# Performance work log

Measured on AMD Instinct MI355X. Metric: run time of the kernel, lower is better.

Reference implementation:

```python
import jax, jax.numpy as jnp
import numpy as np

N_INPUT, N_HIDDEN, N_OUTPUT = 64, 512, 24

def setup_inputs() -> dict:
    key = jax.random.key(0)
    ks = jax.random.split(key, 7)
    s_ih = 1.0 / np.sqrt(N_HIDDEN)
    x = jax.random.normal(ks[0], (256, 512, N_INPUT), dtype=jnp.float32)
    W_ih = jax.random.uniform(ks[1], (N_HIDDEN, N_INPUT), minval=-s_ih, maxval=s_ih, dtype=jnp.float32)
    W_hh = jax.random.uniform(ks[2], (N_HIDDEN, N_HIDDEN), minval=-s_ih, maxval=s_ih, dtype=jnp.float32)
    b_ih = jax.random.uniform(ks[3], (N_HIDDEN,), minval=-s_ih, maxval=s_ih, dtype=jnp.float32)
    b_hh = jax.random.uniform(ks[4], (N_HIDDEN,), minval=-s_ih, maxval=s_ih, dtype=jnp.float32)
    W_ho = jax.random.uniform(ks[5], (N_OUTPUT, N_HIDDEN), minval=-s_ih, maxval=s_ih, dtype=jnp.float32)
    b_ho = jax.random.uniform(ks[6], (N_OUTPUT,), minval=-s_ih, maxval=s_ih, dtype=jnp.float32)
    return {"x": x, "W_ih": W_ih, "W_hh": W_hh, "b_ih": b_ih, "b_hh": b_hh, "W_ho": W_ho, "b_ho": b_ho}

def reference(x, W_ih, W_hh, b_ih, b_hh, W_ho, b_ho):
    B = x.shape[0]
    # Precompute input projections for all timesteps in one big GEMM: [B,T,H]
    xp = jnp.einsum('bti,hi->bth', x, W_ih) + b_ih + b_hh
    h0 = jnp.zeros((B, W_hh.shape[0]), dtype=x.dtype)

    def step(h, xp_t):
        h = jnp.tanh(xp_t + h @ W_hh.T)
        out = jnp.tanh(h @ W_ho.T + b_ho)
        return h, out

    _, outs = jax.lax.scan(step, h0, jnp.swapaxes(xp, 0, 1))  # outs: [T,B,O]
    return jnp.swapaxes(outs, 0, 1)  # [B,T,O]
```

## Files before the change

kernel.cpp:

```cpp
#include <hip/hip_runtime.h>
#include <cstdint>
#include <cstddef>


#define TSTEPS 512
#define HDIM   512
#define NIN    64
#define NOUT   24
#define BB     16
#define HPAD   520
#define XPAD   72
#define KHALF  256
#define HPAD2  264
#define NREG   49
#define NLDS   (64 - NREG)

typedef _Float16 h16;
typedef __attribute__((ext_vector_type(8))) _Float16 h16x8;
typedef __attribute__((ext_vector_type(4))) _Float16 h16x4;
typedef __attribute__((ext_vector_type(2))) _Float16 h16x2;
typedef __attribute__((ext_vector_type(4))) float    f32x4;
typedef __attribute__((ext_vector_type(2))) float    f32x2;

__device__ __forceinline__ float fast_tanh(float z) {
  float e = __builtin_amdgcn_exp2f(z * 2.8853900817779268f);
  return 1.0f - 2.0f * __builtin_amdgcn_rcpf(e + 1.0f);
}

__device__ __forceinline__ h16x8 cvt8(const float* __restrict__ p) {
  f32x4 f0 = *(const f32x4*)p;
  f32x4 f1 = *(const f32x4*)(p + 4);
  h16x8 a;
  #pragma unroll
  for (int j = 0; j < 4; ++j) { a[j] = (h16)f0[j]; a[4 + j] = (h16)f1[j]; }
  return a;
}

__global__ __launch_bounds__(512)
void xp_gemm(const float* __restrict__ x, const float* __restrict__ Wih,
             const float* __restrict__ bih, const float* __restrict__ bhh,
             h16* __restrict__ xp, unsigned* __restrict__ cnt)
{
  const int tid  = threadIdx.x;
  const int wave = tid >> 6;
  const int lane = tid & 63;
  const int lr   = lane & 15;
  const int lk   = lane >> 4;
  const int blk  = blockIdx.x & 15;
  const int tc   = blockIdx.x >> 4;
  const int c0   = wave * 64;

  if (cnt && blockIdx.x == 0 && tid < 64) cnt[tid] = 0u;

  h16x8 A[4][2];
  #pragma unroll
  for (int m = 0; m < 4; ++m)
    #pragma unroll
    for (int s = 0; s < 2; ++s)
      A[m][s] = cvt8(Wih + (size_t)(c0 + 16 * m + lr) * NIN + 32 * s + 8 * lk);

  f32x4 bias[4];
  #pragma unroll
  for (int m = 0; m < 4; ++m) {
    const int c = c0 + 16 * m + 4 * lk;
    f32x4 bi = *(const f32x4*)&bih[c];
    f32x4 bh = *(const f32x4*)&bhh[c];
    bias[m] = bi + bh;
  }

  const float* xrow = x + (size_t)(16 * blk + lr) * (TSTEPS * NIN);

  for (int j = 0; j < 32; ++j) {
    const int t = tc * 32 + j;
    f32x4 acc[4];
    #pragma unroll
    for (int m = 0; m < 4; ++m) acc[m] = bias[m];
    #pragma unroll
    for (int s = 0; s < 2; ++s) {
      h16x8 bx = cvt8(xrow + (size_t)t * NIN + 32 * s + 8 * lk);
      #pragma unroll
      for (int m = 0; m < 4; ++m)
        acc[m] = __builtin_amdgcn_mfma_f32_16x16x32_f16(A[m][s], bx, acc[m], 0, 0, 0);
    }
    h16x8 c0v, c1v;
    #pragma unroll
    for (int i = 0; i < 4; ++i) {
      c0v[i]     = (h16)acc[0][i];
      c0v[4 + i] = (h16)acc[1][i];
      c1v[i]     = (h16)acc[2][i];
      c1v[4 + i] = (h16)acc[3][i];
    }
    h16* p = xp + ((((size_t)t * 16 + blk) * 8 + wave) * 64 + lane) * 16;
    *(h16x8*)p       = c0v;
    *(h16x8*)(p + 8) = c1v;
  }
}

__global__ __launch_bounds__(512, 2)
void rnn_core2(const float* __restrict__ Whh, const h16* __restrict__ xp,
               h16* __restrict__ hall, float* __restrict__ ex,
               unsigned* __restrict__ cnt)
{
  __shared__ h16 hl[2][16 * HPAD2];

  const int tid  = threadIdx.x;
  const int wave = tid >> 6;
  const int lane = tid & 63;
  const int lr   = lane & 15;
  const int lk   = lane >> 4;
  const int kb   = blockIdx.x >> 4;
  const int g    = blockIdx.x & 15;
  const int wq   = wave & 3;
  const bool fin = ((wave >> 2) == kb);
  const int b0   = g * 16;

  h16x8 areg[8][4];
  #pragma unroll
  for (int s = 0; s < 8; ++s)
    #pragma unroll
    for (int m = 0; m < 4; ++m)
      areg[s][m] = cvt8(Whh + (size_t)(64 * wave + 16 * m + lr) * HDIM
                        + KHALF * kb + 32 * s + 8 * lk);

  for (int idx = tid; idx < 16 * HPAD2; idx += 512) hl[0][idx] = (h16)0.f;
  __syncthreads();

  h16x8 xr0, xr1;
  if (fin) {
    const h16* p = xp + (((size_t)g * 8 + wave) * 64 + lane) * 16;
    xr0 = *(const h16x8*)p;
    xr1 = *(const h16x8*)(p + 8);
  }

  unsigned* mycnt   = &cnt[g * 2 + kb];
  unsigned* partcnt = &cnt[g * 2 + (1 - kb)];

  for (int t = 0; t < TSTEPS; ++t) {
    f32x4 acc[4];
    if (fin) {
      #pragma unroll
      for (int i = 0; i < 4; ++i) {
        acc[0][i] = (float)xr0[i];
        acc[1][i] = (float)xr0[4 + i];
        acc[2][i] = (float)xr1[i];
        acc[3][i] = (float)xr1[4 + i];
      }
      const int tn = (t + 1 < TSTEPS) ? (t + 1) : t;
      const h16* p = xp + ((((size_t)tn * 16 + g) * 8 + wave) * 64 + lane) * 16;
      xr0 = *(const h16x8*)p;
      xr1 = *(const h16x8*)(p + 8);
    } else {
      #pragma unroll
      for (int m = 0; m < 4; ++m) { acc[m][0]=0.f; acc[m][1]=0.f; acc[m][2]=0.f; acc[m][3]=0.f; }
    }

    const h16* hb = hl[t & 1];
    #pragma unroll
    for (int s = 0; s < 8; ++s) {
      h16x8 bh = *(const h16x8*)&hb[lr * HPAD2 + 32 * s + 8 * lk];
      #pragma unroll
      for (int m = 0; m < 4; ++m)
        acc[m] = __builtin_amdgcn_mfma_f32_16x16x32_f16(areg[s][m], bh, acc[m], 0, 0, 0);
    }

    if (!fin) {
      float* exw = ex + ((size_t)((g * 2 + kb) * 2 + (t & 1)) << 12);
      #pragma unroll
      for (int m = 0; m < 4; ++m)
        *(f32x4*)&exw[((wq * 16 + m * 4 + lk) << 6) + lr * 4] = acc[m];
      if (lane == 0)
        __hip_atomic_fetch_add(mycnt, 1u, __ATOMIC_RELEASE, __HIP_MEMORY_SCOPE_AGENT);
    } else {
      const unsigned tgt = 4u * (unsigned)(t + 1);
      while (__hip_atomic_load(partcnt, __ATOMIC_ACQUIRE, __HIP_MEMORY_SCOPE_AGENT) < tgt)
        __builtin_amdgcn_s_sleep(1);
      const float* exr = ex + ((size_t)((g * 2 + (1 - kb)) * 2 + (t & 1)) << 12);
      h16* hn   = hl[(t + 1) & 1];
      h16* hrow = hall + ((size_t)t * 256 + b0 + lr) * HDIM + KHALF * kb + 64 * wq + 4 * lk;
      #pragma unroll
      for (int m = 0; m < 4; ++m) {
        f32x4 pp = *(const f32x4*)&exr[((wq * 16 + m * 4 + lk) << 6) + lr * 4];
        h16x4 hv;
        #pragma unroll
        for (int i = 0; i < 4; ++i) hv[i] = (h16)fast_tanh(acc[m][i] + pp[i]);
        *(h16x4*)&hn[lr * HPAD2 + 64 * wq + 16 * m + 4 * lk] = hv;
        *(h16x4*)(hrow + 16 * m) = hv;
      }
    }

    __syncthreads();
  }
}

__global__ __launch_bounds__(512)
void out_all(const h16* __restrict__ hall, const float* __restrict__ Who,
             const float* __restrict__ bho, float* __restrict__ out)
{
  __shared__ h16 wholds[NOUT * HPAD];

  const int tid  = threadIdx.x;
  const int wave = tid >> 6;
  const int lane = tid & 63;
  const int lr   = lane & 15;
  const int lk   = lane >> 4;

  for (int idx = tid; idx < NOUT * HDIM; idx += 512) {
    int r = idx >> 9, k = idx & 511;
    wholds[r * HPAD + k] = (h16)Who[idx];
  }

  f32x4 o0, o1;
  { o0 = *(const f32x4*)&bho[lk * 4]; }
  { int ob = 16 + lk * 4;
    if (ob < NOUT) o1 = *(const f32x4*)&bho[ob];
    else { o1[0] = 0.f; o1[1] = 0.f; o1[2] = 0.f; o1[3] = 0.f; } }
  __syncthreads();

  const int rt = blockIdx.x * 8 + wave;
  const int t  = rt >> 4;
  const int b  = (rt & 15) * 16 + lr;
  const int row1 = (16 + lr < NOUT) ? (16 + lr) : (8 + lr);

  const h16* hrow = hall + ((size_t)t * 256 + b) * HDIM + lk * 8;

  #pragma unroll
  for (int s = 0; s < 16; ++s) {
    h16x8 bh = *(const h16x8*)(hrow + 32 * s);
    h16x8 a0 = *(const h16x8*)&wholds[lr * HPAD + s * 32 + lk * 8];
    h16x8 a1 = *(const h16x8*)&wholds[row1 * HPAD + s * 32 + lk * 8];
    o0 = __builtin_amdgcn_mfma_f32_16x16x32_f16(a0, bh, o0, 0, 0, 0);
    o1 = __builtin_amdgcn_mfma_f32_16x16x32_f16(a1, bh, o1, 0, 0, 0);
  }

  float* op = out + ((size_t)b * TSTEPS + t) * NOUT;
  f32x4 v0;
  #pragma unroll
  for (int i = 0; i < 4; ++i) v0[i] = fast_tanh(o0[i]);
  *(f32x4*)(op + lk * 4) = v0;
  if (lk < 2) {
    f32x4 v1;
    #pragma unroll
    for (int i = 0; i < 4; ++i) v1[i] = fast_tanh(o1[i]);
    *(f32x4*)(op + 16 + lk * 4) = v1;
  }
}

__global__ __launch_bounds__(512, 2)
void rnn_core(const float* __restrict__ Whh, const h16* __restrict__ xp,
              h16* __restrict__ hall)
{
  __shared__ h16 hbuf[2][BB * HPAD];
  __shared__ h16 aslice[NLDS * 8 * 512];

  const int tid  = threadIdx.x;
  const int wave = tid >> 6;
  const int lane = tid & 63;
  const int lr   = lane & 15;
  const int lk   = lane >> 4;
  const int blk  = blockIdx.x;
  const int b0   = blk * BB;
  const int wc0  = wave * 64;

  h16x8 areg[NREG];
  #pragma unroll
  for (int s = 0; s < 16; ++s) {
    #pragma unroll
    for (int m = 0; m < 4; ++m) {
      h16x8 a = cvt8(Whh + (size_t)(wc0 + 16 * m + lr) * HDIM + 32 * s + 8 * lk);
      const int id = s * 4 + m;
      if (id < NREG) areg[id] = a;
      else *(h16x8*)&aslice[(size_t)((id - NREG) * 8 + wave) * 512 + lane * 8] = a;
    }
  }

  for (int idx = tid; idx < BB * HPAD; idx += 512) hbuf[0][idx] = (h16)0.f;
  __syncthreads();

  h16x8 xr0, xr1;
  {
    const h16* p = xp + (((size_t)blk * 8 + wave) * 64 + lane) * 16;
    xr0 = *(const h16x8*)p;
    xr1 = *(const h16x8*)(p + 8);
  }

  for (int t = 0; t < TSTEPS; ++t) {
    const h16* hb = hbuf[t & 1];
    h16*       hn = hbuf[(t + 1) & 1];

    f32x4 acc[4];
    #pragma unroll
    for (int i = 0; i < 4; ++i) {
      acc[0][i] = (float)xr0[i];
      acc[1][i] = (float)xr0[4 + i];
      acc[2][i] = (float)xr1[i];
      acc[3][i] = (float)xr1[4 + i];
    }
    {
      const int tn = (t + 1 < TSTEPS) ? (t + 1) : t;
      const h16* p = xp + ((((size_t)tn * 16 + blk) * 8 + wave) * 64 + lane) * 16;
      xr0 = *(const h16x8*)p;
      xr1 = *(const h16x8*)(p + 8);
    }

    #pragma unroll
    for (int s = 0; s < 16; ++s) {
      h16x8 bh = *(const h16x8*)&hb[lr * HPAD + 32 * s + 8 * lk];
      #pragma unroll
      for (int m = 0; m < 4; ++m) {
        const int id = s * 4 + m;
        h16x8 a = (id < NREG)
            ? areg[id]
            : *(const h16x8*)&aslice[(size_t)((id - NREG) * 8 + wave) * 512 + lane * 8];
        acc[m] = __builtin_amdgcn_mfma_f32_16x16x32_f16(a, bh, acc[m], 0, 0, 0);
      }
    }

    h16* hrow = hall + ((size_t)t * 256 + b0 + lr) * HDIM + wc0 + lk * 4;
    #pragma unroll
    for (int m = 0; m < 4; ++m) {
      h16x4 hv;
      #pragma unroll
      for (int i = 0; i < 4; ++i) hv[i] = (h16)fast_tanh(acc[m][i]);
      *(h16x4*)&hn[lr * HPAD + wc0 + 16 * m + 4 * lk] = hv;
      *(h16x4*)(hrow + 16 * m) = hv;
    }

    __syncthreads();
  }
}

__device__ __forceinline__ void out_proj(
    int t, const h16* __restrict__ hb, const h16* __restrict__ who,
    f32x4 bho0, f32x4 bho1, float* __restrict__ out, int b0, int lr, int lk)
{
  f32x4 o0 = bho0, o1 = bho1;
  const int row1 = (16 + lr < NOUT) ? (16 + lr) : (8 + lr);
  #pragma unroll
  for (int s = 0; s < 16; ++s) {
    h16x8 bh = *(const h16x8*)&hb[lr * HPAD + s * 32 + lk * 8];
    h16x8 a0 = *(const h16x8*)&who[lr * HPAD + s * 32 + lk * 8];
    h16x8 a1 = *(const h16x8*)&who[row1 * HPAD + s * 32 + lk * 8];
    o0 = __builtin_amdgcn_mfma_f32_16x16x32_f16(a0, bh, o0, 0, 0, 0);
    o1 = __builtin_amdgcn_mfma_f32_16x16x32_f16(a1, bh, o1, 0, 0, 0);
  }
  float* op = out + ((size_t)(b0 + lr) * TSTEPS + t) * NOUT;
  f32x4 v0;
  #pragma unroll
  for (int i = 0; i < 4; ++i) v0[i] = fast_tanh(o0[i]);
  *(f32x4*)(op + lk * 4) = v0;
  if (lk < 2) {
    f32x4 v1;
    #pragma unroll
    for (int i = 0; i < 4; ++i) v1[i] = fast_tanh(o1[i]);
    *(f32x4*)(op + 16 + lk * 4) = v1;
  }
}

__global__ __launch_bounds__(512, 2)
void rnn_fused(const float* __restrict__ x,
               const float* __restrict__ Wih,
               const float* __restrict__ Whh,
               const float* __restrict__ bih,
               const float* __restrict__ bhh,
               const float* __restrict__ Who,
               const float* __restrict__ bho,
               float* __restrict__ out)
{
  __shared__ h16 hbuf[2][BB * HPAD];
  __shared__ h16 xbuf[2][BB * XPAD];
  __shared__ h16 wholds[NOUT * HPAD];

  const int tid  = threadIdx.x;
  const int wave = tid >> 6;
  const int lane = tid & 63;
  const int lr   = lane & 15;
  const int lk   = lane >> 4;
  const int b0   = blockIdx.x * BB;
  const int wc0  = wave * 64;

  h16x8 a_rec[4][16];
  #pragma unroll
  for (int m = 0; m < 4; ++m) {
    const int row = wc0 + m * 16 + lr;
    #pragma unroll
    for (int s = 0; s < 16; ++s)
      a_rec[m][s] = cvt8(Whh + (size_t)row * HDIM + s * 32 + lk * 8);
  }
  h16x8 a_ih[4][2];
  #pragma unroll
  for (int m = 0; m < 4; ++m) {
    const int row = wc0 + m * 16 + lr;
    #pragma unroll
    for (int s = 0; s < 2; ++s)
      a_ih[m][s] = cvt8(Wih + (size_t)row * NIN + s * 32 + lk * 8);
  }
  f32x4 biasv[4];
  #pragma unroll
  for (int m = 0; m < 4; ++m) {
    const int c = wc0 + m * 16 + lk * 4;
    f32x4 bi = *(const f32x4*)&bih[c];
    f32x4 bh2 = *(const f32x4*)&bhh[c];
    biasv[m] = bi + bh2;
  }
  f32x4 bho0, bho1;
  { bho0 = *(const f32x4*)&bho[lk * 4]; }
  { int ob = 16 + lk * 4;
    if (ob < NOUT) bho1 = *(const f32x4*)&bho[ob];
    else { bho1[0] = 0.f; bho1[1] = 0.f; bho1[2] = 0.f; bho1[3] = 0.f; } }

  for (int idx = tid; idx < NOUT * HDIM; idx += 512) {
    int r = idx >> 9, k = idx & 511;
    wholds[r * HPAD + k] = (h16)Who[idx];
  }
  for (int idx = tid; idx < BB * HPAD; idx += 512) hbuf[0][idx] = (h16)0.f;
  {
    int r = tid >> 5, c2 = (tid & 31) * 2;
    f32x2 v = *(const f32x2*)(x + ((size_t)(b0 + r) * TSTEPS + 0) * NIN + c2);
    h16x2 pk = { (h16)v.x, (h16)v.y };
    *(h16x2*)&xbuf[0][r * XPAD + c2] = pk;
  }
  __syncthreads();

  for (int t = 0; t < TSTEPS; ++t) {
    const h16* hb = hbuf[t & 1];
    h16*       hn = hbuf[(t + 1) & 1];
    const h16* xb = xbuf[t & 1];
    h16*       xn = xbuf[(t + 1) & 1];

    if (t > 0 && wave == ((t - 1) & 7))
      out_proj(t - 1, hb, wholds, bho0, bho1, out, b0, lr, lk);

    const int tl = (t + 1 < TSTEPS) ? (t + 1) : (TSTEPS - 1);
    const int xr = tid >> 5, xc = (tid & 31) * 2;
    f32x2 xv = *(const f32x2*)(x + ((size_t)(b0 + xr) * TSTEPS + tl) * NIN + xc);

    f32x4 acc[4];
    #pragma unroll
    for (int m = 0; m < 4; ++m) acc[m] = biasv[m];
    #pragma unroll
    for (int s = 0; s < 2; ++s) {
      h16x8 bx = *(const h16x8*)&xb[lr * XPAD + s * 32 + lk * 8];
      #pragma unroll
      for (int m = 0; m < 4; ++m)
        acc[m] = __builtin_amdgcn_mfma_f32_16x16x32_f16(a_ih[m][s], bx, acc[m], 0, 0, 0);
    }
    #pragma unroll
    for (int s = 0; s < 16; ++s) {
      h16x8 bh = *(const h16x8*)&hb[lr * HPAD + 32 * s + 8 * lk];
      #pragma unroll
      for (int m = 0; m < 4; ++m)
        acc[m] = __builtin_amdgcn_mfma_f32_16x16x32_f16(a_rec[m][s], bh, acc[m], 0, 0, 0);
    }
    #pragma unroll
    for (int m = 0; m < 4; ++m) {
      h16x4 hv;
      #pragma unroll
      for (int i = 0; i < 4; ++i) hv[i] = (h16)fast_tanh(acc[m][i]);
      *(h16x4*)&hn[lr * HPAD + wc0 + 16 * m + 4 * lk] = hv;
    }
    {
      h16x2 pk = { (h16)xv.x, (h16)xv.y };
      *(h16x2*)&xn[xr * XPAD + xc] = pk;
    }
    __syncthreads();
  }

  if (wave == ((TSTEPS - 1) & 7))
    out_proj(TSTEPS - 1, hbuf[TSTEPS & 1], wholds, bho0, bho1, out, b0, lr, lk);
}

extern "C" void kernel_launch(void* const* d_in, const int* in_sizes, int n_in,
                              void* d_out, int out_size, void* d_ws, size_t ws_size,
                              hipStream_t stream) {
  (void)in_sizes; (void)n_in; (void)out_size;
  const float* x   = (const float*)d_in[0];
  const float* Wih = (const float*)d_in[1];
  const float* Whh = (const float*)d_in[2];
  const float* bih = (const float*)d_in[3];
  const float* bhh = (const float*)d_in[4];
  const float* Who = (const float*)d_in[5];
  const float* bho = (const float*)d_in[6];
  float* out = (float*)d_out;

  const size_t XP_BYTES   = (size_t)TSTEPS * 256 * HDIM * sizeof(h16);
  const size_t HALL_BYTES = (size_t)TSTEPS * 256 * HDIM * sizeof(h16);
  const size_t EX_BYTES   = (size_t)64 * 4096 * sizeof(float);
  const size_t CNT_BYTES  = 64 * sizeof(unsigned);

  if (ws_size >= XP_BYTES + HALL_BYTES + EX_BYTES + CNT_BYTES) {
    h16*      xp   = (h16*)d_ws;
    h16*      hall = (h16*)((char*)d_ws + XP_BYTES);
    float*    ex   = (float*)((char*)d_ws + XP_BYTES + HALL_BYTES);
    unsigned* cnt  = (unsigned*)((char*)d_ws + XP_BYTES + HALL_BYTES + EX_BYTES);
    xp_gemm<<<dim3(256), dim3(512), 0, stream>>>(x, Wih, bih, bhh, xp, cnt);
    rnn_core2<<<dim3(32), dim3(512), 0, stream>>>(Whh, xp, hall, ex, cnt);
    out_all<<<dim3(1024), dim3(512), 0, stream>>>(hall, Who, bho, out);
  } else if (ws_size >= XP_BYTES + HALL_BYTES) {
    h16* xp   = (h16*)d_ws;
    h16* hall = (h16*)((char*)d_ws + XP_BYTES);
    xp_gemm<<<dim3(256), dim3(512), 0, stream>>>(x, Wih, bih, bhh, xp, nullptr);
    rnn_core<<<dim3(256 / BB), dim3(512), 0, stream>>>(Whh, xp, hall);
    out_all<<<dim3(1024), dim3(512), 0, stream>>>(hall, Who, bho, out);
  } else {
    rnn_fused<<<dim3(256 / BB), dim3(512), 0, stream>>>(x, Wih, Whh, bih, bhh, Who, bho, out);
  }
}
```

Measured before the change: 1.090 ms.

## Place exchange scratch in output tail and defer per-step hidden-state stores

The cross-block exchange buffer and sync counters for the split-K recurrence kernel now live in the tail of the output buffer instead of the workspace. This lets the two-block-per-group path run whenever the workspace holds only xp and hall. That tail is later fully overwritten by the output projection kernel. The global store of each step's hidden state is also deferred to the start of the next step, taking that store off the critical path before the barrier. The trade-off is that correctness now relies on the output buffer being large enough and on the kernels running in stream order.

```diff
diff --git a/kernel.cpp b/kernel.cpp
--- a/kernel.cpp
+++ b/kernel.cpp
@@ -14,6 +14,8 @@
 #define HPAD2  264
 #define NREG   49
 #define NLDS   (64 - NREG)
+#define EX_F32  (64 * 4096)
+#define CNT_U32 64
 
 typedef _Float16 h16;
 typedef __attribute__((ext_vector_type(8))) _Float16 h16x8;
@@ -50,7 +52,7 @@
   const int tc   = blockIdx.x >> 4;
   const int c0   = wave * 64;
 
-  if (cnt && blockIdx.x == 0 && tid < 64) cnt[tid] = 0u;
+  if (cnt && blockIdx.x == 0 && tid < CNT_U32) cnt[tid] = 0u;
 
   h16x8 A[4][2];
   #pragma unroll
@@ -135,7 +137,16 @@
   unsigned* mycnt   = &cnt[g * 2 + kb];
   unsigned* partcnt = &cnt[g * 2 + (1 - kb)];
 
+  h16x4 pend[4];
+  h16*  pendRow = hall;
+
   for (int t = 0; t < TSTEPS; ++t) {
+    if (fin && t > 0) {
+      #pragma unroll
+      for (int m = 0; m < 4; ++m)
+        *(h16x4*)(pendRow + 16 * m) = pend[m];
+    }
+
     f32x4 acc[4];
     if (fin) {
       #pragma unroll
@@ -175,8 +186,7 @@
       while (__hip_atomic_load(partcnt, __ATOMIC_ACQUIRE, __HIP_MEMORY_SCOPE_AGENT) < tgt)
         __builtin_amdgcn_s_sleep(1);
       const float* exr = ex + ((size_t)((g * 2 + (1 - kb)) * 2 + (t & 1)) << 12);
-      h16* hn   = hl[(t + 1) & 1];
-      h16* hrow = hall + ((size_t)t * 256 + b0 + lr) * HDIM + KHALF * kb + 64 * wq + 4 * lk;
+      h16* hn = hl[(t + 1) & 1];
       #pragma unroll
       for (int m = 0; m < 4; ++m) {
         f32x4 pp = *(const f32x4*)&exr[((wq * 16 + m * 4 + lk) << 6) + lr * 4];
@@ -184,11 +194,18 @@
         #pragma unroll
         for (int i = 0; i < 4; ++i) hv[i] = (h16)fast_tanh(acc[m][i] + pp[i]);
         *(h16x4*)&hn[lr * HPAD2 + 64 * wq + 16 * m + 4 * lk] = hv;
-        *(h16x4*)(hrow + 16 * m) = hv;
+        pend[m] = hv;
       }
+      pendRow = hall + ((size_t)t * 256 + b0 + lr) * HDIM + KHALF * kb + 64 * wq + 4 * lk;
     }
 
     __syncthreads();
+  }
+
+  if (fin) {
+    #pragma unroll
+    for (int m = 0; m < 4; ++m)
+      *(h16x4*)(pendRow + 16 * m) = pend[m];
   }
 }
 
@@ -472,7 +489,7 @@
 extern "C" void kernel_launch(void* const* d_in, const int* in_sizes, int n_in,
                               void* d_out, int out_size, void* d_ws, size_t ws_size,
                               hipStream_t stream) {
-  (void)in_sizes; (void)n_in; (void)out_size;
+  (void)in_sizes; (void)n_in;
   const float* x   = (const float*)d_in[0];
   const float* Wih = (const float*)d_in[1];
   const float* Whh = (const float*)d_in[2];
@@ -484,14 +501,13 @@
 
   const size_t XP_BYTES   = (size_t)TSTEPS * 256 * HDIM * sizeof(h16);
   const size_t HALL_BYTES = (size_t)TSTEPS * 256 * HDIM * sizeof(h16);
-  const size_t EX_BYTES   = (size_t)64 * 4096 * sizeof(float);
-  const size_t CNT_BYTES  = 64 * sizeof(unsigned);
-
-  if (ws_size >= XP_BYTES + HALL_BYTES + EX_BYTES + CNT_BYTES) {
+  const int    EX_TAIL    = EX_F32 + CNT_U32;
+
+  if (ws_size >= XP_BYTES + HALL_BYTES && out_size >= EX_TAIL + 16) {
     h16*      xp   = (h16*)d_ws;
     h16*      hall = (h16*)((char*)d_ws + XP_BYTES);
-    float*    ex   = (float*)((char*)d_ws + XP_BYTES + HALL_BYTES);
-    unsigned* cnt  = (unsigned*)((char*)d_ws + XP_BYTES + HALL_BYTES + EX_BYTES);
+    float*    ex   = out + ((size_t)out_size - EX_TAIL);
+    unsigned* cnt  = (unsigned*)(ex + EX_F32);
     xp_gemm<<<dim3(256), dim3(512), 0, stream>>>(x, Wih, bih, bhh, xp, cnt);
     rnn_core2<<<dim3(32), dim3(512), 0, stream>>>(Whh, xp, hall, ex, cnt);
     out_all<<<dim3(1024), dim3(512), 0, stream>>>(hall, Who, bho, out);
```

Measured after the change: 3.759 ms. 245% more time.
